# Optimization experiments

Measured on AMD Instinct MI355X. Metric: run time of the kernel, lower is better.

## Reference

```python
import jax, jax.numpy as jnp
import numpy as np
import math

D_IN = 1024
D_MODEL = 1024
NHEAD = 16
HEAD_SIZE = D_MODEL // NHEAD  # 64; used only for the softmax scale
B, SQ, SKV = 8, 2048, 2048


def setup_inputs() -> dict:
    key = jax.random.key(0)
    ks = jax.random.split(key, 8)
    s = 1.0 / math.sqrt(D_IN)
    return {
        "hidden_states": jax.random.normal(ks[0], (B, SQ, D_IN), jnp.float32),
        "encoder_hidden_states": jax.random.normal(ks[1], (B, SKV, D_IN), jnp.float32),
        "Wq": jax.random.normal(ks[2], (D_IN, D_MODEL), jnp.float32) * s,
        "bq": jnp.zeros((D_MODEL,), jnp.float32),
        "Wk": jax.random.normal(ks[3], (D_IN, D_MODEL), jnp.float32) * s,
        "bk": jnp.zeros((D_MODEL,), jnp.float32),
        "Wv": jax.random.normal(ks[4], (D_IN, D_MODEL), jnp.float32) * s,
        "bv": jnp.zeros((D_MODEL,), jnp.float32),
    }


def reference(hidden_states, encoder_hidden_states, Wq, bq, Wk, bk, Wv, bv):
    # QKV projections: [B, S, d_in] @ [d_in, d_model]
    Q = hidden_states @ Wq + bq                 # [B, SQ, D]
    K = encoder_hidden_states @ Wk + bk         # [B, SKV, D]
    V = encoder_hidden_states @ Wv + bv         # [B, SKV, D]
    # NOTE: original module does NOT split heads; scale uses head_size.
    scores = jnp.einsum('bqd,bkd->bqk', Q, K) / math.sqrt(HEAD_SIZE)
    probs = jax.nn.softmax(scores, axis=-1)     # [B, SQ, SKV]
    return jnp.einsum('bqk,bkd->bqd', probs, V)  # [B, SQ, D]
```

## Files before the change

### kernel.cpp

```cpp
#include <hip/hip_runtime.h>

typedef _Float16 half8 __attribute__((ext_vector_type(8)));
typedef _Float16 half4 __attribute__((ext_vector_type(4)));
typedef float f32x4 __attribute__((ext_vector_type(4)));

#define AS1 __attribute__((address_space(1)))
#define AS3 __attribute__((address_space(3)))

__global__ __launch_bounds__(256) void cvt2_kernel(const float* __restrict__ H, const float* __restrict__ E,
                                                   _Float16* __restrict__ Hh, _Float16* __restrict__ Eh, int n4) {
    const float4* s4 = (const float4*)(blockIdx.z ? E : H);
    half4* d4 = (half4*)(blockIdx.z ? Eh : Hh);
    int i = blockIdx.x * blockDim.x + threadIdx.x;
    int stride = gridDim.x * blockDim.x;
    for (; i < n4; i += stride) {
        float4 f = s4[i];
        half4 o;
        o.x = (_Float16)f.x; o.y = (_Float16)f.y; o.z = (_Float16)f.z; o.w = (_Float16)f.w;
        d4[i] = o;
    }
}

__global__ __launch_bounds__(256) void wtrans_kernel(const float* __restrict__ W0, const float* __restrict__ W1,
                                                     const float* __restrict__ W2,
                                                     _Float16* __restrict__ T0, _Float16* __restrict__ T1,
                                                     _Float16* __restrict__ T2) {
    const float* W = blockIdx.z == 0 ? W0 : (blockIdx.z == 1 ? W1 : W2);
    _Float16* T = blockIdx.z == 0 ? T0 : (blockIdx.z == 1 ? T1 : T2);
    __shared__ float tile[32][33];
    int tx = threadIdx.x & 31, tg = threadIdx.x >> 5;
    int k0 = blockIdx.y * 32, n0 = blockIdx.x * 32;
#pragma unroll
    for (int i = 0; i < 4; i++) tile[tg + i * 8][tx] = W[(long)(k0 + tg + i * 8) * 1024 + n0 + tx];
    __syncthreads();
#pragma unroll
    for (int i = 0; i < 4; i++) T[(long)(n0 + tg + i * 8) * 1024 + k0 + tx] = (_Float16)tile[tx][tg + i * 8];
}

__device__ __forceinline__ void gemm_core(const _Float16* __restrict__ Ab, int lda,
                                          const _Float16* __restrict__ Bb, int ldb, int K,
                                          _Float16* sA, _Float16* sB, f32x4 acc[4][4]) {
    const int tid = threadIdx.x;
    const int wv = tid >> 6, lane = tid & 63;
    const int wr = wv >> 1, wc = wv & 1;
    const int quad = lane >> 4, l16 = lane & 15;
    const int srow = lane >> 2;
    const int g = ((lane & 3) ^ ((srow >> 1) & 3)) * 8;
    const int rc = (quad ^ ((l16 >> 1) & 3)) * 8;
    const int c0 = wv * 2;

    for (int k0 = 0; k0 < K; k0 += 32) {
#pragma unroll
        for (int c = c0; c < c0 + 2; ++c) {
            int row = c * 16 + srow;
            __builtin_amdgcn_global_load_lds((const AS1 void*)(Ab + (long)row * lda + k0 + g),
                                             (AS3 void*)(&sA[c * 512]), 16, 0, 0);
            __builtin_amdgcn_global_load_lds((const AS1 void*)(Bb + (long)row * ldb + k0 + g),
                                             (AS3 void*)(&sB[c * 512]), 16, 0, 0);
        }
        __syncthreads();
        half8 af[4], bfr[4];
#pragma unroll
        for (int mi = 0; mi < 4; mi++) af[mi] = *(const half8*)&sA[(wr * 64 + mi * 16 + l16) * 32 + rc];
#pragma unroll
        for (int ni = 0; ni < 4; ni++) bfr[ni] = *(const half8*)&sB[(wc * 64 + ni * 16 + l16) * 32 + rc];
#pragma unroll
        for (int mi = 0; mi < 4; mi++)
#pragma unroll
            for (int ni = 0; ni < 4; ni++)
                acc[mi][ni] = __builtin_amdgcn_mfma_f32_16x16x32_f16(af[mi], bfr[ni], acc[mi][ni], 0, 0, 0);
        __syncthreads();
    }
}

struct QkvParams {
    const _Float16 *Hh, *Eh, *WqT, *WkT, *WvT;
    const float *bq, *bk, *bv;
    _Float16 *Qh, *Kh, *Vt;
};

__global__ __launch_bounds__(256, 4) void qkv_kernel(QkvParams p) {
    __shared__ __align__(16) _Float16 sA[128 * 32];
    __shared__ __align__(16) _Float16 sB[128 * 32];
    const int b = blockIdx.x;
    const int xcd = b & 7, s = b >> 3;
    const int z = s >> 7;
    const int r = s & 127;
    const int by = xcd + ((r >> 3) << 3);
    const int bx = r & 7;

    const _Float16* A  = (z == 0) ? p.Hh : p.Eh;
    const _Float16* Bt = (z == 0) ? p.WqT : (z == 1 ? p.WkT : p.WvT);
    const float* bias  = (z == 0) ? p.bq : (z == 1 ? p.bk : p.bv);
    const _Float16* Ab = A + (long)(by * 128) * 1024;
    const _Float16* Bb = Bt + (long)(bx * 128) * 1024;

    f32x4 acc[4][4];
#pragma unroll
    for (int i = 0; i < 4; i++)
#pragma unroll
        for (int j = 0; j < 4; j++) acc[i][j] = {0.f, 0.f, 0.f, 0.f};
    gemm_core(Ab, 1024, Bb, 1024, 1024, sA, sB, acc);

    const int wv = threadIdx.x >> 6, lane = threadIdx.x & 63;
    const int wr = wv >> 1, wc = wv & 1;
    const int quad = lane >> 4, l16 = lane & 15;
    const int m_base = by * 128 + wr * 64 + quad * 4;
    const int n_base = bx * 128 + wc * 64 + l16;

    if (z < 2) {
        _Float16* C = (z == 0) ? p.Qh : p.Kh;
#pragma unroll
        for (int mi = 0; mi < 4; mi++)
#pragma unroll
            for (int ni = 0; ni < 4; ni++) {
                int n = n_base + ni * 16;
                float bv_ = bias[n];
#pragma unroll
                for (int r2 = 0; r2 < 4; r2++)
                    C[(long)(m_base + mi * 16 + r2) * 1024 + n] = (_Float16)(acc[mi][ni][r2] + bv_);
            }
    } else {
        _Float16* C = p.Vt;
#pragma unroll
        for (int mi = 0; mi < 4; mi++) {
            int m0 = m_base + mi * 16;
            long bb = m0 >> 11;
            int t = m0 & 2047;
#pragma unroll
            for (int ni = 0; ni < 4; ni++) {
                int n = n_base + ni * 16;
                float bv_ = bias[n];
                half4 o;
                o.x = (_Float16)(acc[mi][ni][0] + bv_);
                o.y = (_Float16)(acc[mi][ni][1] + bv_);
                o.z = (_Float16)(acc[mi][ni][2] + bv_);
                o.w = (_Float16)(acc[mi][ni][3] + bv_);
                *(half4*)&C[bb * (1024L * 2048) + (long)n * 2048 + t] = o;
            }
        }
    }
}

template <int OUTK, int GXLOG>
__global__ __launch_bounds__(256, 4) void gemm_bt(const _Float16* __restrict__ A, long bsA, int lda,
                                                  const _Float16* __restrict__ Bt, long bsB, int ldb,
                                                  void* __restrict__ Cv, long bsC, int ldc,
                                                  float scale, int K) {
    __shared__ __align__(16) _Float16 sA[128 * 32];
    __shared__ __align__(16) _Float16 sB[128 * 32];
    const int b = blockIdx.x;
    const long zb = b & 7;
    const int s = b >> 3;
    const int bx = s & ((1 << GXLOG) - 1);
    const int by = s >> GXLOG;

    const _Float16* Ab = A + zb * bsA + (long)(by * 128) * lda;
    const _Float16* Bb = Bt + zb * bsB + (long)(bx * 128) * ldb;

    f32x4 acc[4][4];
#pragma unroll
    for (int i = 0; i < 4; i++)
#pragma unroll
        for (int j = 0; j < 4; j++) acc[i][j] = {0.f, 0.f, 0.f, 0.f};
    gemm_core(Ab, lda, Bb, ldb, K, sA, sB, acc);

    const int wv = threadIdx.x >> 6, lane = threadIdx.x & 63;
    const int wr = wv >> 1, wc = wv & 1;
    const int quad = lane >> 4, l16 = lane & 15;
    const int m_base = by * 128 + wr * 64 + quad * 4;
    const int n_base = bx * 128 + wc * 64 + l16;

    if (OUTK == 0) {
        _Float16* C = (_Float16*)Cv + zb * bsC;
#pragma unroll
        for (int mi = 0; mi < 4; mi++)
#pragma unroll
            for (int ni = 0; ni < 4; ni++) {
                int n = n_base + ni * 16;
#pragma unroll
                for (int r = 0; r < 4; r++)
                    C[(long)(m_base + mi * 16 + r) * ldc + n] = (_Float16)(acc[mi][ni][r] * scale);
            }
    } else {
        float* C = (float*)Cv + zb * bsC;
#pragma unroll
        for (int mi = 0; mi < 4; mi++)
#pragma unroll
            for (int ni = 0; ni < 4; ni++) {
                int n = n_base + ni * 16;
#pragma unroll
                for (int r = 0; r < 4; r++)
                    C[(long)(m_base + mi * 16 + r) * ldc + n] = acc[mi][ni][r];
            }
    }
}

__global__ __launch_bounds__(256) void softmax_kernel(_Float16* __restrict__ S) {
    const long row = blockIdx.x;
    _Float16* p = S + row * 2048;
    half8 raw = ((const half8*)p)[threadIdx.x];
    float v[8];
#pragma unroll
    for (int i = 0; i < 8; i++) v[i] = (float)raw[i];

    float mx = v[0];
#pragma unroll
    for (int i = 1; i < 8; i++) mx = fmaxf(mx, v[i]);
#pragma unroll
    for (int off = 32; off > 0; off >>= 1) mx = fmaxf(mx, __shfl_xor(mx, off, 64));
    __shared__ float redm[4], reds[4];
    int lane = threadIdx.x & 63, w = threadIdx.x >> 6;
    if (lane == 0) redm[w] = mx;
    __syncthreads();
    mx = fmaxf(fmaxf(redm[0], redm[1]), fmaxf(redm[2], redm[3]));

    float e[8], sum = 0.f;
#pragma unroll
    for (int i = 0; i < 8; i++) { e[i] = __expf(v[i] - mx); sum += e[i]; }
#pragma unroll
    for (int off = 32; off > 0; off >>= 1) sum += __shfl_xor(sum, off, 64);
    if (lane == 0) reds[w] = sum;
    __syncthreads();
    sum = reds[0] + reds[1] + reds[2] + reds[3];
    float inv = 1.0f / sum;

    half8 o;
#pragma unroll
    for (int i = 0; i < 8; i++) o[i] = (_Float16)(e[i] * inv);
    ((half8*)p)[threadIdx.x] = o;
}

extern "C" void kernel_launch(void* const* d_in, const int* in_sizes, int n_in,
                              void* d_out, int out_size, void* d_ws, size_t ws_size,
                              hipStream_t stream) {
    const float* H  = (const float*)d_in[0];
    const float* E  = (const float*)d_in[1];
    const float* Wq = (const float*)d_in[2];
    const float* bq = (const float*)d_in[3];
    const float* Wk = (const float*)d_in[4];
    const float* bk = (const float*)d_in[5];
    const float* Wv = (const float*)d_in[6];
    const float* bv = (const float*)d_in[7];
    float* out = (float*)d_out;

    char* ws = (char*)d_ws;
    _Float16* Hh  = (_Float16*)(ws + 0L);
    _Float16* Eh  = (_Float16*)(ws + 33554432L);
    _Float16* WqT = (_Float16*)(ws + 67108864L);
    _Float16* WkT = (_Float16*)(ws + 69206016L);
    _Float16* WvT = (_Float16*)(ws + 71303168L);
    _Float16* Qh  = (_Float16*)(ws + 73400320L);
    _Float16* Kh  = (_Float16*)(ws + 106954752L);
    _Float16* Vt  = (_Float16*)(ws + 140509184L);
    _Float16* S   = (_Float16*)(ws + 174063616L);

    cvt2_kernel<<<dim3(2048, 1, 2), 256, 0, stream>>>(H, E, Hh, Eh, 16384 * 1024 / 4);
    wtrans_kernel<<<dim3(32, 32, 3), 256, 0, stream>>>(Wq, Wk, Wv, WqT, WkT, WvT);
    QkvParams qp{Hh, Eh, WqT, WkT, WvT, bq, bk, bv, Qh, Kh, Vt};
    qkv_kernel<<<3072, 256, 0, stream>>>(qp);
    gemm_bt<0, 4><<<2048, 256, 0, stream>>>(Qh, 2048L * 1024, 1024, Kh, 2048L * 1024, 1024,
                                            (void*)S, 2048L * 2048, 2048, 0.125f, 1024);
    softmax_kernel<<<16384, 256, 0, stream>>>(S);
    gemm_bt<1, 3><<<1024, 256, 0, stream>>>(S, 2048L * 2048, 2048, Vt, 1024L * 2048, 2048,
                                            (void*)out, 2048L * 1024, 1024, 1.f, 2048);
    (void)in_sizes; (void)n_in; (void)out_size; (void)ws_size;
}
```

Before: 481.8 us.

## Double GEMM K-tile to 64 with new XOR swizzle for LDS layout

Raises the shared GEMM core's K step from 32 to 64, loading 128x64 fp16 tiles of A and B into LDS with an 8-way XOR swizzle and issuing two MFMAs per accumulator per iteration. This halves the number of barrier pairs and loop iterations per GEMM and gives more MFMA work between syncs. In exchange LDS per block doubles to 32 KB and launch bounds drop to 3 blocks per CU, which lowers occupancy.

Result: faster. 451.8 us (-6.2%).

```diff
diff --git a/kernel.cpp b/kernel.cpp
--- a/kernel.cpp
+++ b/kernel.cpp
@@ -44,31 +44,40 @@
     const int wv = tid >> 6, lane = tid & 63;
     const int wr = wv >> 1, wc = wv & 1;
     const int quad = lane >> 4, l16 = lane & 15;
-    const int srow = lane >> 2;
-    const int g = ((lane & 3) ^ ((srow >> 1) & 3)) * 8;
-    const int rc = (quad ^ ((l16 >> 1) & 3)) * 8;
-    const int c0 = wv * 2;
-
-    for (int k0 = 0; k0 < K; k0 += 32) {
-#pragma unroll
-        for (int c = c0; c < c0 + 2; ++c) {
-            int row = c * 16 + srow;
-            __builtin_amdgcn_global_load_lds((const AS1 void*)(Ab + (long)row * lda + k0 + g),
-                                             (AS3 void*)(&sA[c * 512]), 16, 0, 0);
-            __builtin_amdgcn_global_load_lds((const AS1 void*)(Bb + (long)row * ldb + k0 + g),
-                                             (AS3 void*)(&sB[c * 512]), 16, 0, 0);
+    const int srow_g = lane >> 3;
+    const int sclog = ((lane & 7) ^ srow_g) * 8;
+    const int p0 = (quad ^ (l16 & 7)) * 8;
+
+    for (int k0 = 0; k0 < K; k0 += 64) {
+#pragma unroll
+        for (int i = 0; i < 4; i++) {
+            int row = wv * 32 + i * 8;
+            __builtin_amdgcn_global_load_lds((const AS1 void*)(Ab + (long)(row + srow_g) * lda + k0 + sclog),
+                                             (AS3 void*)(&sA[row * 64]), 16, 0, 0);
+            __builtin_amdgcn_global_load_lds((const AS1 void*)(Bb + (long)(row + srow_g) * ldb + k0 + sclog),
+                                             (AS3 void*)(&sB[row * 64]), 16, 0, 0);
         }
         __syncthreads();
-        half8 af[4], bfr[4];
-#pragma unroll
-        for (int mi = 0; mi < 4; mi++) af[mi] = *(const half8*)&sA[(wr * 64 + mi * 16 + l16) * 32 + rc];
-#pragma unroll
-        for (int ni = 0; ni < 4; ni++) bfr[ni] = *(const half8*)&sB[(wc * 64 + ni * 16 + l16) * 32 + rc];
-#pragma unroll
-        for (int mi = 0; mi < 4; mi++)
-#pragma unroll
-            for (int ni = 0; ni < 4; ni++)
-                acc[mi][ni] = __builtin_amdgcn_mfma_f32_16x16x32_f16(af[mi], bfr[ni], acc[mi][ni], 0, 0, 0);
+        half8 af[4][2], bf[4][2];
+#pragma unroll
+        for (int mi = 0; mi < 4; mi++) {
+            int r = (wr * 64 + mi * 16 + l16) * 64;
+            af[mi][0] = *(const half8*)&sA[r + p0];
+            af[mi][1] = *(const half8*)&sA[r + (p0 ^ 32)];
+        }
+#pragma unroll
+        for (int ni = 0; ni < 4; ni++) {
+            int r = (wc * 64 + ni * 16 + l16) * 64;
+            bf[ni][0] = *(const half8*)&sB[r + p0];
+            bf[ni][1] = *(const half8*)&sB[r + (p0 ^ 32)];
+        }
+#pragma unroll
+        for (int mi = 0; mi < 4; mi++)
+#pragma unroll
+            for (int ni = 0; ni < 4; ni++) {
+                acc[mi][ni] = __builtin_amdgcn_mfma_f32_16x16x32_f16(af[mi][0], bf[ni][0], acc[mi][ni], 0, 0, 0);
+                acc[mi][ni] = __builtin_amdgcn_mfma_f32_16x16x32_f16(af[mi][1], bf[ni][1], acc[mi][ni], 0, 0, 0);
+            }
         __syncthreads();
     }
 }
@@ -79,9 +88,9 @@
     _Float16 *Qh, *Kh, *Vt;
 };
 
-__global__ __launch_bounds__(256, 4) void qkv_kernel(QkvParams p) {
-    __shared__ __align__(16) _Float16 sA[128 * 32];
-    __shared__ __align__(16) _Float16 sB[128 * 32];
+__global__ __launch_bounds__(256, 3) void qkv_kernel(QkvParams p) {
+    __shared__ __align__(16) _Float16 sA[128 * 64];
+    __shared__ __align__(16) _Float16 sB[128 * 64];
     const int b = blockIdx.x;
     const int xcd = b & 7, s = b >> 3;
     const int z = s >> 7;
@@ -143,12 +152,12 @@
 }
 
 template <int OUTK, int GXLOG>
-__global__ __launch_bounds__(256, 4) void gemm_bt(const _Float16* __restrict__ A, long bsA, int lda,
+__global__ __launch_bounds__(256, 3) void gemm_bt(const _Float16* __restrict__ A, long bsA, int lda,
                                                   const _Float16* __restrict__ Bt, long bsB, int ldb,
                                                   void* __restrict__ Cv, long bsC, int ldc,
                                                   float scale, int K) {
-    __shared__ __align__(16) _Float16 sA[128 * 32];
-    __shared__ __align__(16) _Float16 sB[128 * 32];
+    __shared__ __align__(16) _Float16 sA[128 * 64];
+    __shared__ __align__(16) _Float16 sB[128 * 64];
     const int b = blockIdx.x;
     const long zb = b & 7;
     const int s = b >> 3;
```
